# Kernel tuning notes

Hardware: AMD Instinct MI355X
Metric: run time of the kernel (lower is better)

## Reference

```python
import jax, jax.numpy as jnp
import numpy as np

TF = 512  # text_features
VF = 512  # video_features


def setup_inputs() -> dict:
    key = jax.random.key(0)
    k1, k2, k3 = jax.random.split(key, 3)
    text = jax.random.normal(k1, (4, 32, TF), dtype=jnp.float32)
    video = jax.random.normal(k2, (4, 64, 196, VF), dtype=jnp.float32)
    # nn.Linear(text_features + video_features, 1): weight (1, TF+VF), bias (1,)
    w = jax.random.normal(k3, (TF + VF,), dtype=jnp.float32) * (1.0 / np.sqrt(TF + VF))
    b = jnp.zeros((1,), dtype=jnp.float32)
    return {"text": text, "video": video, "w": w, "b": b}


def reference(text, video, w, b):
    # Split the 1-output linear over the concat into text-only and video-only
    # projections: Linear(cat([t, v])) = t @ wt + v @ wv + b  (exact algebra).
    tf = text.shape[-1]
    wt, wv = w[:tf], w[tf:]
    score_t = jnp.einsum('btf,f->bt', text, wt) + b[0]        # (B, St)
    score_v = jnp.einsum('bvhf,f->bvh', video, wv)            # (B, Sv, HW)
    scores = score_t[:, :, None, None] + score_v[:, None]     # (B, St, Sv, HW)
    B, St, Sv, HW = scores.shape
    # softmax over the flattened (Sv*HW) dim, per (b, st)
    weights = jax.nn.softmax(scores.reshape(B, St, Sv * HW), axis=-1)
    weights = weights.reshape(B, St, Sv, HW)
    # fused[b,st,sv,f] = sum_hw weights[b,st,sv,hw] * video[b,sv,hw,f]
    fused = jnp.einsum('bsvh,bvhf->bsvf', weights, video)
    return fused
```

## Files before the change

kernel.cpp:

```cpp
#include <hip/hip_runtime.h>

#define TF 512
#define VF 512
#define BB 4
#define ST 32
#define SV 64
#define HW 196
#define NBV (BB * SV)
#define NSEG 4
#define SEGH (HW / NSEG)


__global__ __launch_bounds__(256) void score_acc_kernel(const float4* __restrict__ video,
                                                        const float* __restrict__ w,
                                                        float4* __restrict__ Gpart,
                                                        float* __restrict__ dpart) {
    int bv   = blockIdx.x >> 2;
    int seg  = blockIdx.x & 3;
    int tid  = threadIdx.x;
    int wave = tid >> 6;
    int lane = tid & 63;

    const float4* wv4 = (const float4*)(w + TF);
    float4 w0 = wv4[lane];
    float4 w1 = wv4[lane + 64];

    const float4* vbase = video + ((size_t)bv * HW + seg * SEGH) * (VF / 4);

    float4 acc0 = make_float4(0.f, 0.f, 0.f, 0.f);
    float4 acc1 = make_float4(0.f, 0.f, 0.f, 0.f);
    float  esum = 0.f;

    #pragma unroll 2
    for (int hl = wave; hl < SEGH; hl += 4) {
        const float4* row = vbase + hl * (VF / 4);
        float4 x0 = row[lane];
        float4 x1 = row[lane + 64];
        float s = x0.x * w0.x + x0.y * w0.y + x0.z * w0.z + x0.w * w0.w
                + x1.x * w1.x + x1.y * w1.y + x1.z * w1.z + x1.w * w1.w;
        #pragma unroll
        for (int off = 32; off > 0; off >>= 1)
            s += __shfl_xor(s, off, 64);
        float e = __expf(s);
        esum += e;
        acc0.x = fmaf(e, x0.x, acc0.x);
        acc0.y = fmaf(e, x0.y, acc0.y);
        acc0.z = fmaf(e, x0.z, acc0.z);
        acc0.w = fmaf(e, x0.w, acc0.w);
        acc1.x = fmaf(e, x1.x, acc1.x);
        acc1.y = fmaf(e, x1.y, acc1.y);
        acc1.z = fmaf(e, x1.z, acc1.z);
        acc1.w = fmaf(e, x1.w, acc1.w);
    }

    __shared__ float4 sacc[4][VF / 4];
    __shared__ float  sd[4];
    sacc[wave][lane]      = acc0;
    sacc[wave][lane + 64] = acc1;
    if (lane == 0) sd[wave] = esum;
    __syncthreads();

    int c = tid & 127, half = tid >> 7;
    float4 a  = sacc[half * 2][c];
    float4 bq = sacc[half * 2 + 1][c];
    float4 t  = make_float4(a.x + bq.x, a.y + bq.y, a.z + bq.z, a.w + bq.w);
    sacc[half * 2][c] = t;
    __syncthreads();
    if (half == 0) {
        float4 u = sacc[2][c];
        Gpart[((size_t)seg * NBV + bv) * (VF / 4) + c] =
            make_float4(t.x + u.x, t.y + u.y, t.z + u.z, t.w + u.w);
    }
    if (tid == 0) dpart[blockIdx.x] = sd[0] + sd[1] + sd[2] + sd[3];
}

__global__ __launch_bounds__(256) void out_kernel(const float4* __restrict__ Gpart,
                                                  const float* __restrict__ dpart,
                                                  float4* __restrict__ out) {
    int bv  = blockIdx.x;
    int b   = bv >> 6;
    int v   = bv & 63;
    int tid = threadIdx.x;

    __shared__ float  red[4];
    __shared__ float4 gsh[2][VF / 4];

    float val = dpart[b * 256 + tid];
    #pragma unroll
    for (int off = 32; off > 0; off >>= 1) val += __shfl_xor(val, off, 64);
    if ((tid & 63) == 0) red[tid >> 6] = val;

    int c = tid & 127, half = tid >> 7;
    float4 g0 = Gpart[((size_t)(half * 2) * NBV + bv) * (VF / 4) + c];
    float4 g1 = Gpart[((size_t)(half * 2 + 1) * NBV + bv) * (VF / 4) + c];
    gsh[half][c] = make_float4(g0.x + g1.x, g0.y + g1.y, g0.z + g1.z, g0.w + g1.w);
    __syncthreads();

    float inv = 1.0f / (red[0] + red[1] + red[2] + red[3]);
    float4 o0 = gsh[0][c], o1 = gsh[1][c];
    float4 res = make_float4((o0.x + o1.x) * inv, (o0.y + o1.y) * inv,
                             (o0.z + o1.z) * inv, (o0.w + o1.w) * inv);

    #pragma unroll
    for (int k = 0; k < 16; k++) {
        int s = half * 16 + k;
        out[(((size_t)(b * ST + s)) * SV + v) * (VF / 4) + c] = res;
    }
}

extern "C" void kernel_launch(void* const* d_in, const int* in_sizes, int n_in,
                              void* d_out, int out_size, void* d_ws, size_t ws_size,
                              hipStream_t stream) {
    const float* video = (const float*)d_in[1];
    const float* w     = (const float*)d_in[2];
    float4* Gpart = (float4*)d_ws;
    float*  dpart = (float*)((char*)d_ws + (size_t)NSEG * NBV * (VF / 4) * sizeof(float4));

    score_acc_kernel<<<NBV * NSEG, 256, 0, stream>>>((const float4*)video, w,
                                                     Gpart, dpart);
    out_kernel<<<NBV, 256, 0, stream>>>(Gpart, dpart, (float4*)d_out);
}
```

Measured before the change: 165.6 us.

## Fuse score and output kernels via cooperative grid sync

Merges the two kernels into one cooperative kernel. A grid-wide sync replaces the kernel boundary, and each of the 1024 blocks then writes a quarter of the broadcast output rows for its (b,v). This removes one launch and spreads the output writes over four times as many blocks. In exchange it adds grid-sync overhead, and all 1024 blocks must be co-resident or the cooperative launch fails.

```diff
diff --git a/kernel.cpp b/kernel.cpp
--- a/kernel.cpp
+++ b/kernel.cpp
@@ -1,4 +1,7 @@
 #include <hip/hip_runtime.h>
+#include <hip/hip_cooperative_groups.h>
+
+namespace cg = cooperative_groups;
 
 #define TF 512
 #define VF 512
@@ -9,14 +12,18 @@
 #define NBV (BB * SV)
 #define NSEG 4
 #define SEGH (HW / NSEG)
+#define NBLK (NBV * NSEG)
 
 
-__global__ __launch_bounds__(256) void score_acc_kernel(const float4* __restrict__ video,
-                                                        const float* __restrict__ w,
-                                                        float4* __restrict__ Gpart,
-                                                        float* __restrict__ dpart) {
+__global__ __launch_bounds__(256) void fused_kernel(const float4* __restrict__ video,
+                                                    const float* __restrict__ w,
+                                                    float4* __restrict__ Gpart,
+                                                    float* __restrict__ dpart,
+                                                    float4* __restrict__ out) {
     int bv   = blockIdx.x >> 2;
     int seg  = blockIdx.x & 3;
+    int b    = bv >> 6;
+    int v    = bv & 63;
     int tid  = threadIdx.x;
     int wave = tid >> 6;
     int lane = tid & 63;
@@ -55,6 +62,7 @@
 
     __shared__ float4 sacc[4][VF / 4];
     __shared__ float  sd[4];
+    __shared__ float  red[4];
     sacc[wave][lane]      = acc0;
     sacc[wave][lane + 64] = acc1;
     if (lane == 0) sd[wave] = esum;
@@ -72,38 +80,28 @@
             make_float4(t.x + u.x, t.y + u.y, t.z + u.z, t.w + u.w);
     }
     if (tid == 0) dpart[blockIdx.x] = sd[0] + sd[1] + sd[2] + sd[3];
-}
 
-__global__ __launch_bounds__(256) void out_kernel(const float4* __restrict__ Gpart,
-                                                  const float* __restrict__ dpart,
-                                                  float4* __restrict__ out) {
-    int bv  = blockIdx.x;
-    int b   = bv >> 6;
-    int v   = bv & 63;
-    int tid = threadIdx.x;
-
-    __shared__ float  red[4];
-    __shared__ float4 gsh[2][VF / 4];
+    cg::this_grid().sync();
 
     float val = dpart[b * 256 + tid];
     #pragma unroll
     for (int off = 32; off > 0; off >>= 1) val += __shfl_xor(val, off, 64);
-    if ((tid & 63) == 0) red[tid >> 6] = val;
+    if (lane == 0) red[wave] = val;
+    __syncthreads();
+    float inv = 1.0f / (red[0] + red[1] + red[2] + red[3]);
 
-    int c = tid & 127, half = tid >> 7;
-    float4 g0 = Gpart[((size_t)(half * 2) * NBV + bv) * (VF / 4) + c];
-    float4 g1 = Gpart[((size_t)(half * 2 + 1) * NBV + bv) * (VF / 4) + c];
-    gsh[half][c] = make_float4(g0.x + g1.x, g0.y + g1.y, g0.z + g1.z, g0.w + g1.w);
-    __syncthreads();
-
-    float inv = 1.0f / (red[0] + red[1] + red[2] + red[3]);
-    float4 o0 = gsh[0][c], o1 = gsh[1][c];
-    float4 res = make_float4((o0.x + o1.x) * inv, (o0.y + o1.y) * inv,
-                             (o0.z + o1.z) * inv, (o0.w + o1.w) * inv);
+    float4 g0 = Gpart[((size_t)0 * NBV + bv) * (VF / 4) + c];
+    float4 g1 = Gpart[((size_t)1 * NBV + bv) * (VF / 4) + c];
+    float4 g2 = Gpart[((size_t)2 * NBV + bv) * (VF / 4) + c];
+    float4 g3 = Gpart[((size_t)3 * NBV + bv) * (VF / 4) + c];
+    float4 res = make_float4((g0.x + g1.x + g2.x + g3.x) * inv,
+                             (g0.y + g1.y + g2.y + g3.y) * inv,
+                             (g0.z + g1.z + g2.z + g3.z) * inv,
+                             (g0.w + g1.w + g2.w + g3.w) * inv);
 
     #pragma unroll
-    for (int k = 0; k < 16; k++) {
-        int s = half * 16 + k;
+    for (int k = 0; k < 4; k++) {
+        int s = seg * 8 + half * 4 + k;
         out[(((size_t)(b * ST + s)) * SV + v) * (VF / 4) + c] = res;
     }
 }
@@ -111,12 +109,13 @@
 extern "C" void kernel_launch(void* const* d_in, const int* in_sizes, int n_in,
                               void* d_out, int out_size, void* d_ws, size_t ws_size,
                               hipStream_t stream) {
-    const float* video = (const float*)d_in[1];
-    const float* w     = (const float*)d_in[2];
+    const float4* video = (const float4*)d_in[1];
+    const float*  w     = (const float*)d_in[2];
     float4* Gpart = (float4*)d_ws;
     float*  dpart = (float*)((char*)d_ws + (size_t)NSEG * NBV * (VF / 4) * sizeof(float4));
+    float4* out   = (float4*)d_out;
 
-    score_acc_kernel<<<NBV * NSEG, 256, 0, stream>>>((const float4*)video, w,
-                                                     Gpart, dpart);
-    out_kernel<<<NBV, 256, 0, stream>>>(Gpart, dpart, (float4*)d_out);
+    void* args[] = {(void*)&video, (void*)&w, (void*)&Gpart, (void*)&dpart, (void*)&out};
+    hipLaunchCooperativeKernel((const void*)fused_kernel, dim3(NBLK), dim3(256),
+                               args, 0, stream);
 }
```

Result: slower. 241.6 us (+45.9%).
